# Kernel optimization log

Hardware: AMD Instinct MI355X
Metric: run time of the kernel (lower is better)

The kernel has to match this reference:

```python
import jax, jax.numpy as jnp
import numpy as np

N = 262144        # input_size = n_nodes * in_features (n_kernels = 1)
E = 16777216      # number of nonzero (i, j, param_idx) entries in weight_distribution
NPARAMS = 1280    # in_features * n_node_labels^2 * max_distance * n_kernels
NB = 16           # in_features * n_node_labels * n_kernels


def setup_inputs() -> dict:
    key = jax.random.key(0)
    ks = jax.random.split(key, 7)
    return {
        "x": jax.random.normal(ks[0], (N,), jnp.float32),
        "Param_W": jax.random.normal(ks[1], (NPARAMS,), jnp.float32),
        "Param_b": jax.random.normal(ks[2], (NB,), jnp.float32),
        "w_rows": jax.random.randint(ks[3], (E,), 0, N, jnp.int32),
        "w_cols": jax.random.randint(ks[4], (E,), 0, N, jnp.int32),
        "w_params": jax.random.randint(ks[5], (E,), 0, NPARAMS, jnp.int32),
        "b_params": jax.random.randint(ks[6], (N,), 0, NB, jnp.int32),
    }


def reference(x, Param_W, Param_b, w_rows, w_cols, w_params, b_params):
    # Original: W[i, j] = Param_W[p] for every (i, j, p) in weight_distribution,
    # then out = W @ x + bias. Fused gather-scale-scatter avoids materializing W.
    vals = Param_W[w_params] * x[w_cols]              # [E]
    out = jax.ops.segment_sum(vals, w_rows, num_segments=N)  # [N]
    # bias[i] = Param_b[b_params[i]] (one shared bias per output position)
    return out + Param_b[b_params]
```

## Files before the change

kernel.cpp:

```cpp
#include <hip/hip_runtime.h>


#define SLICE_BITS  15
#define SLICE_SIZE  (1 << SLICE_BITS)
#define SLICES      8
#define CHUNKS      32
#define NPARAMS_MAX 2048
#define SCAN_THREADS 1024
#define SB4         4
#define VB          4

typedef float v4f __attribute__((ext_vector_type(4)));

__global__ __launch_bounds__(256) void val_kernel(
    const float* __restrict__ x, const float* __restrict__ PW, int nparams,
    const int4* __restrict__ cols4, const int4* __restrict__ params4,
    v4f* __restrict__ vals4)
{
    __shared__ float pw[NPARAMS_MAX];
    for (int j = threadIdx.x; j < nparams; j += 256) pw[j] = PW[j];
    __syncthreads();
    const int base = blockIdx.x * (256 * VB) + threadIdx.x;
    int4 c[VB], p[VB];
#pragma unroll
    for (int k = 0; k < VB; ++k) {
        c[k] = cols4[base + k * 256];
        p[k] = params4[base + k * 256];
    }
#pragma unroll
    for (int k = 0; k < VB; ++k) {
        v4f v;
        v.x = pw[p[k].x] * x[c[k].x];
        v.y = pw[p[k].y] * x[c[k].y];
        v.z = pw[p[k].z] * x[c[k].z];
        v.w = pw[p[k].w] * x[c[k].w];
        __builtin_nontemporal_store(v, &vals4[base + k * 256]);
    }
}

__global__ __launch_bounds__(SCAN_THREADS, 1) void scan4_kernel(
    const int4* __restrict__ rows4, const float4* __restrict__ vals4,
    float* __restrict__ partials, int e4_per_chunk)
{
    __shared__ float acc[SLICE_SIZE];
    const int bid = blockIdx.x;
    const int s = bid / CHUNKS;
    const int c = bid % CHUNKS;
    for (int j = threadIdx.x; j < SLICE_SIZE; j += SCAN_THREADS) acc[j] = 0.0f;
    __syncthreads();

    const int4*   rp = rows4 + (size_t)c * e4_per_chunk;
    const float4* vp = vals4 + (size_t)c * e4_per_chunk;
    const int per_thread = e4_per_chunk / SCAN_THREADS;

    int4   rA[SB4], rB[SB4];
    float4 vA[SB4], vB[SB4];

#define LOAD(dstR, dstV, b0)                                             \
    _Pragma("unroll")                                                    \
    for (int b = 0; b < SB4; ++b) {                                      \
        const int g = ((b0) + b) * SCAN_THREADS + threadIdx.x;           \
        dstR[b] = rp[g];                                                 \
        dstV[b] = vp[g];                                                 \
    }
#define PROC(rX, vX)                                                     \
    _Pragma("unroll")                                                    \
    for (int b = 0; b < SB4; ++b) {                                      \
        if ((rX[b].x >> SLICE_BITS) == s) atomicAdd(&acc[rX[b].x & (SLICE_SIZE - 1)], vX[b].x); \
        if ((rX[b].y >> SLICE_BITS) == s) atomicAdd(&acc[rX[b].y & (SLICE_SIZE - 1)], vX[b].y); \
        if ((rX[b].z >> SLICE_BITS) == s) atomicAdd(&acc[rX[b].z & (SLICE_SIZE - 1)], vX[b].z); \
        if ((rX[b].w >> SLICE_BITS) == s) atomicAdd(&acc[rX[b].w & (SLICE_SIZE - 1)], vX[b].w); \
    }

    LOAD(rA, vA, 0)
    for (int base = 0; base < per_thread; base += 2 * SB4) {
        LOAD(rB, vB, base + SB4)
        PROC(rA, vA)
        if (base + 2 * SB4 < per_thread) {
            LOAD(rA, vA, base + 2 * SB4)
        }
        PROC(rB, vB)
    }
#undef LOAD
#undef PROC
    __syncthreads();

    float* dst = partials + (size_t)bid * SLICE_SIZE;
    for (int j = threadIdx.x; j < SLICE_SIZE; j += SCAN_THREADS) dst[j] = acc[j];
}

__global__ __launch_bounds__(256) void reduce_bias_kernel(
    const float* __restrict__ partials, const float* __restrict__ Pb,
    const int* __restrict__ bp, float* __restrict__ out, int n)
{
    const int i = blockIdx.x * 256 + threadIdx.x;
    if (i >= n) return;
    const int s = i >> SLICE_BITS;
    const int j = i & (SLICE_SIZE - 1);
    const float* p = partials + ((size_t)s * CHUNKS) * SLICE_SIZE + j;
    float sum = 0.0f;
#pragma unroll
    for (int g = 0; g < CHUNKS; ++g) sum += p[(size_t)g * SLICE_SIZE];
    out[i] = sum + Pb[bp[i]];
}

#define FB_BATCH 4
__global__ __launch_bounds__(SCAN_THREADS, 1) void slice_scan_kernel(
    const float* __restrict__ x, const float* __restrict__ PW, int nparams,
    const int4* __restrict__ rows4, const int4* __restrict__ cols4,
    const int4* __restrict__ params4, float* __restrict__ partials,
    int e4_per_chunk)
{
    __shared__ float acc[SLICE_SIZE];
    __shared__ float pw_lds[NPARAMS_MAX];
    const int bid = blockIdx.x;
    const int s = bid / CHUNKS;
    const int c = bid % CHUNKS;
    for (int j = threadIdx.x; j < SLICE_SIZE; j += SCAN_THREADS) acc[j] = 0.0f;
    for (int j = threadIdx.x; j < nparams; j += SCAN_THREADS) pw_lds[j] = PW[j];
    __syncthreads();
    const int4* rp = rows4   + (size_t)c * e4_per_chunk;
    const int4* cp = cols4   + (size_t)c * e4_per_chunk;
    const int4* qp = params4 + (size_t)c * e4_per_chunk;
    const int per_thread = e4_per_chunk / SCAN_THREADS;
    for (int base = 0; base < per_thread; base += FB_BATCH) {
        int4 r[FB_BATCH], cc[FB_BATCH], pp[FB_BATCH];
#pragma unroll
        for (int b = 0; b < FB_BATCH; ++b) {
            const int g = (base + b) * SCAN_THREADS + threadIdx.x;
            r[b] = rp[g]; cc[b] = cp[g]; pp[b] = qp[g];
        }
#pragma unroll
        for (int b = 0; b < FB_BATCH; ++b) {
            if ((r[b].x >> SLICE_BITS) == s)
                atomicAdd(&acc[r[b].x & (SLICE_SIZE - 1)], pw_lds[pp[b].x] * x[cc[b].x]);
            if ((r[b].y >> SLICE_BITS) == s)
                atomicAdd(&acc[r[b].y & (SLICE_SIZE - 1)], pw_lds[pp[b].y] * x[cc[b].y]);
            if ((r[b].z >> SLICE_BITS) == s)
                atomicAdd(&acc[r[b].z & (SLICE_SIZE - 1)], pw_lds[pp[b].z] * x[cc[b].z]);
            if ((r[b].w >> SLICE_BITS) == s)
                atomicAdd(&acc[r[b].w & (SLICE_SIZE - 1)], pw_lds[pp[b].w] * x[cc[b].w]);
        }
    }
    __syncthreads();
    float* dst = partials + (size_t)bid * SLICE_SIZE;
    for (int j = threadIdx.x; j < SLICE_SIZE; j += SCAN_THREADS) dst[j] = acc[j];
}

__global__ __launch_bounds__(256) void bias_init_kernel(const float* __restrict__ Pb,
                                                        const int* __restrict__ bp,
                                                        float* __restrict__ out, int n) {
    int i = blockIdx.x * 256 + threadIdx.x;
    if (i < n) out[i] = Pb[bp[i]];
}

__global__ __launch_bounds__(256) void edge_scatter_kernel(const float* __restrict__ x,
                                                           const float* __restrict__ PW,
                                                           const int* __restrict__ rows,
                                                           const int* __restrict__ cols,
                                                           const int* __restrict__ params,
                                                           float* __restrict__ out, int E) {
    int e = blockIdx.x * 256 + threadIdx.x;
    if (e < E) atomicAdd(out + rows[e], PW[params[e]] * x[cols[e]]);
}

extern "C" void kernel_launch(void* const* d_in, const int* in_sizes, int n_in,
                              void* d_out, int out_size, void* d_ws, size_t ws_size,
                              hipStream_t stream) {
    const float* x        = (const float*)d_in[0];
    const float* Param_W  = (const float*)d_in[1];
    const float* Param_b  = (const float*)d_in[2];
    const int*   w_rows   = (const int*)d_in[3];
    const int*   w_cols   = (const int*)d_in[4];
    const int*   w_params = (const int*)d_in[5];
    const int*   b_params = (const int*)d_in[6];
    float* out = (float*)d_out;

    const int N_  = in_sizes[0];
    const int NP_ = in_sizes[1];
    const int E_  = in_sizes[3];
    const int e4  = E_ / 4;

    const size_t partial_bytes = (size_t)SLICES * CHUNKS * SLICE_SIZE * sizeof(float);
    const size_t vals_bytes    = (size_t)E_ * sizeof(float);
    const bool shapes_ok = (N_ == SLICES * SLICE_SIZE) && (NP_ <= NPARAMS_MAX) &&
                           (E_ % (4 * 256 * VB) == 0) &&
                           (E_ % (4 * CHUNKS * SCAN_THREADS * 2 * SB4) == 0);

    if (shapes_ok && ws_size >= vals_bytes + partial_bytes) {
        float*  vals     = (float*)d_ws;
        float*  partials = (float*)((char*)d_ws + vals_bytes);
        const int e4_per_chunk = e4 / CHUNKS;
        val_kernel<<<e4 / (256 * VB), 256, 0, stream>>>(
            x, Param_W, NP_, (const int4*)w_cols, (const int4*)w_params, (v4f*)vals);
        scan4_kernel<<<SLICES * CHUNKS, SCAN_THREADS, 0, stream>>>(
            (const int4*)w_rows, (const float4*)vals, partials, e4_per_chunk);
        reduce_bias_kernel<<<(N_ + 255) / 256, 256, 0, stream>>>(
            partials, Param_b, b_params, out, N_);
    } else if ((N_ == SLICES * SLICE_SIZE) && (NP_ <= NPARAMS_MAX) &&
               (E_ % (4 * CHUNKS * SCAN_THREADS * FB_BATCH) == 0) &&
               ws_size >= partial_bytes) {
        float* partials = (float*)d_ws;
        const int e4_per_chunk = e4 / CHUNKS;
        slice_scan_kernel<<<SLICES * CHUNKS, SCAN_THREADS, 0, stream>>>(
            x, Param_W, NP_, (const int4*)w_rows, (const int4*)w_cols,
            (const int4*)w_params, partials, e4_per_chunk);
        reduce_bias_kernel<<<(N_ + 255) / 256, 256, 0, stream>>>(
            partials, Param_b, b_params, out, N_);
    } else {
        bias_init_kernel<<<(N_ + 255) / 256, 256, 0, stream>>>(Param_b, b_params, out, N_);
        edge_scatter_kernel<<<(E_ + 255) / 256, 256, 0, stream>>>(
            x, Param_W, w_rows, w_cols, w_params, out, E_);
    }
}
```

Baseline: 330.4 us.

## Overlap second-half value computation with first-half slice scan in merged kernel

Splits the edge list in half. The first half's values are computed by val_kernel. A merged kernel then has half its threads scan the first half into shared-memory slice accumulators while the other half computes values for the second half, and scan4_kernel finishes the second half by accumulating into the partials. The aim is to hide the val_kernel's gather and memory traffic behind the scan's LDS atomics. The cost is an extra read-modify-write of the partials buffer and an extra kernel launch, and the merged kernel reads PW from global memory instead of shared.

```diff
diff --git a/kernel.cpp b/kernel.cpp
--- a/kernel.cpp
+++ b/kernel.cpp
@@ -9,6 +9,9 @@
 #define SCAN_THREADS 1024
 #define SB4         4
 #define VB          4
+#define M_SCAN_T    512
+#define M_VAL_T     512
+#define M_THREADS   1024
 
 typedef float v4f __attribute__((ext_vector_type(4)));
 
@@ -40,7 +43,7 @@
 
 __global__ __launch_bounds__(SCAN_THREADS, 1) void scan4_kernel(
     const int4* __restrict__ rows4, const float4* __restrict__ vals4,
-    float* __restrict__ partials, int e4_per_chunk)
+    float* __restrict__ partials, int e4_per_chunk, int accumulate)
 {
     __shared__ float acc[SLICE_SIZE];
     const int bid = blockIdx.x;
@@ -59,7 +62,7 @@
 #define LOAD(dstR, dstV, b0)                                             \
     _Pragma("unroll")                                                    \
     for (int b = 0; b < SB4; ++b) {                                      \
-        const int g = ((b0) + b) * SCAN_THREADS + threadIdx.x;           \
+        const int g = ((b0) + b) * SCAN_THREADS + (int)threadIdx.x;      \
         dstR[b] = rp[g];                                                 \
         dstV[b] = vp[g];                                                 \
     }
@@ -86,7 +89,89 @@
     __syncthreads();
 
     float* dst = partials + (size_t)bid * SLICE_SIZE;
-    for (int j = threadIdx.x; j < SLICE_SIZE; j += SCAN_THREADS) dst[j] = acc[j];
+    if (accumulate) {
+        for (int j = threadIdx.x; j < SLICE_SIZE; j += SCAN_THREADS) dst[j] += acc[j];
+    } else {
+        for (int j = threadIdx.x; j < SLICE_SIZE; j += SCAN_THREADS) dst[j] = acc[j];
+    }
+}
+
+__global__ __launch_bounds__(M_THREADS, 1) void merged_kernel(
+    const int4* __restrict__ rows4, const float4* __restrict__ vals4,
+    float* __restrict__ partials, int e4_per_chunk,
+    const float* __restrict__ x, const float* __restrict__ PW,
+    const int4* __restrict__ cols4v, const int4* __restrict__ params4v,
+    v4f* __restrict__ vals4v, int vpt)
+{
+    __shared__ float acc[SLICE_SIZE];
+    const int bid = blockIdx.x;
+    const int s = bid / CHUNKS;
+    const int c = bid % CHUNKS;
+    for (int j = threadIdx.x; j < SLICE_SIZE; j += M_THREADS) acc[j] = 0.0f;
+    __syncthreads();
+
+    if (threadIdx.x < M_SCAN_T) {
+        const int4*   rp = rows4 + (size_t)c * e4_per_chunk;
+        const float4* vp = vals4 + (size_t)c * e4_per_chunk;
+        const int per_thread = e4_per_chunk / M_SCAN_T;
+
+        int4   rA[SB4], rB[SB4];
+        float4 vA[SB4], vB[SB4];
+
+#define MLOAD(dstR, dstV, b0)                                            \
+    _Pragma("unroll")                                                    \
+    for (int b = 0; b < SB4; ++b) {                                      \
+        const int g = ((b0) + b) * M_SCAN_T + (int)threadIdx.x;          \
+        dstR[b] = rp[g];                                                 \
+        dstV[b] = vp[g];                                                 \
+    }
+#define MPROC(rX, vX)                                                    \
+    _Pragma("unroll")                                                    \
+    for (int b = 0; b < SB4; ++b) {                                      \
+        if ((rX[b].x >> SLICE_BITS) == s) atomicAdd(&acc[rX[b].x & (SLICE_SIZE - 1)], vX[b].x); \
+        if ((rX[b].y >> SLICE_BITS) == s) atomicAdd(&acc[rX[b].y & (SLICE_SIZE - 1)], vX[b].y); \
+        if ((rX[b].z >> SLICE_BITS) == s) atomicAdd(&acc[rX[b].z & (SLICE_SIZE - 1)], vX[b].z); \
+        if ((rX[b].w >> SLICE_BITS) == s) atomicAdd(&acc[rX[b].w & (SLICE_SIZE - 1)], vX[b].w); \
+    }
+
+        MLOAD(rA, vA, 0)
+        for (int base = 0; base < per_thread; base += 2 * SB4) {
+            MLOAD(rB, vB, base + SB4)
+            MPROC(rA, vA)
+            if (base + 2 * SB4 < per_thread) {
+                MLOAD(rA, vA, base + 2 * SB4)
+            }
+            MPROC(rB, vB)
+        }
+#undef MLOAD
+#undef MPROC
+    } else {
+        const int vtid = (int)threadIdx.x - M_SCAN_T;
+        const size_t blockBase = (size_t)bid * vpt * M_VAL_T;
+        for (int k = 0; k < vpt; k += 4) {
+            int4 cc[4], pp[4];
+#pragma unroll
+            for (int u = 0; u < 4; ++u) {
+                const size_t g = blockBase + (size_t)(k + u) * M_VAL_T + vtid;
+                cc[u] = cols4v[g];
+                pp[u] = params4v[g];
+            }
+#pragma unroll
+            for (int u = 0; u < 4; ++u) {
+                const size_t g = blockBase + (size_t)(k + u) * M_VAL_T + vtid;
+                v4f v;
+                v.x = PW[pp[u].x] * x[cc[u].x];
+                v.y = PW[pp[u].y] * x[cc[u].y];
+                v.z = PW[pp[u].z] * x[cc[u].z];
+                v.w = PW[pp[u].w] * x[cc[u].w];
+                __builtin_nontemporal_store(v, &vals4v[g]);
+            }
+        }
+    }
+    __syncthreads();
+
+    float* dst = partials + (size_t)bid * SLICE_SIZE;
+    for (int j = threadIdx.x; j < SLICE_SIZE; j += M_THREADS) dst[j] = acc[j];
 }
 
 __global__ __launch_bounds__(256) void reduce_bias_kernel(
@@ -180,25 +265,52 @@
     const int NP_ = in_sizes[1];
     const int E_  = in_sizes[3];
     const int e4  = E_ / 4;
+    const int e4h = e4 / 2;
 
     const size_t partial_bytes = (size_t)SLICES * CHUNKS * SLICE_SIZE * sizeof(float);
     const size_t vals_bytes    = (size_t)E_ * sizeof(float);
-    const bool shapes_ok = (N_ == SLICES * SLICE_SIZE) && (NP_ <= NPARAMS_MAX) &&
-                           (E_ % (4 * 256 * VB) == 0) &&
-                           (E_ % (4 * CHUNKS * SCAN_THREADS * 2 * SB4) == 0);
-
-    if (shapes_ok && ws_size >= vals_bytes + partial_bytes) {
+
+    const bool base_ok = (N_ == SLICES * SLICE_SIZE) && (NP_ <= NPARAMS_MAX);
+
+    bool split_ok = base_ok && (E_ % 8 == 0) && (e4h % CHUNKS == 0) &&
+                    (e4h % (256 * VB) == 0);
+    const int e4c_h = split_ok ? (e4h / CHUNKS) : 0;
+    const int vpt   = split_ok ? (e4h / (256 * M_VAL_T)) : 0;
+    split_ok = split_ok &&
+               (e4c_h % (M_SCAN_T * 2 * SB4) == 0) &&
+               (e4c_h % (SCAN_THREADS * 2 * SB4) == 0) &&
+               (vpt > 0) && (vpt % 4 == 0) &&
+               ((size_t)256 * M_VAL_T * vpt == (size_t)e4h);
+
+    const bool full_ok = base_ok && (E_ % (4 * 256 * VB) == 0) &&
+                         (E_ % (4 * CHUNKS * SCAN_THREADS * 2 * SB4) == 0);
+
+    if (split_ok && ws_size >= vals_bytes + partial_bytes) {
+        float* vals     = (float*)d_ws;
+        float* partials = (float*)((char*)d_ws + vals_bytes);
+
+        val_kernel<<<e4h / (256 * VB), 256, 0, stream>>>(
+            x, Param_W, NP_, (const int4*)w_cols, (const int4*)w_params, (v4f*)vals);
+        merged_kernel<<<SLICES * CHUNKS, M_THREADS, 0, stream>>>(
+            (const int4*)w_rows, (const float4*)vals, partials, e4c_h,
+            x, Param_W,
+            (const int4*)w_cols + e4h, (const int4*)w_params + e4h,
+            (v4f*)vals + e4h, vpt);
+        scan4_kernel<<<SLICES * CHUNKS, SCAN_THREADS, 0, stream>>>(
+            (const int4*)w_rows + e4h, (const float4*)vals + e4h, partials, e4c_h, 1);
+        reduce_bias_kernel<<<(N_ + 255) / 256, 256, 0, stream>>>(
+            partials, Param_b, b_params, out, N_);
+    } else if (full_ok && ws_size >= vals_bytes + partial_bytes) {
         float*  vals     = (float*)d_ws;
         float*  partials = (float*)((char*)d_ws + vals_bytes);
         const int e4_per_chunk = e4 / CHUNKS;
         val_kernel<<<e4 / (256 * VB), 256, 0, stream>>>(
             x, Param_W, NP_, (const int4*)w_cols, (const int4*)w_params, (v4f*)vals);
         scan4_kernel<<<SLICES * CHUNKS, SCAN_THREADS, 0, stream>>>(
-            (const int4*)w_rows, (const float4*)vals, partials, e4_per_chunk);
+            (const int4*)w_rows, (const float4*)vals, partials, e4_per_chunk, 0);
         reduce_bias_kernel<<<(N_ + 255) / 256, 256, 0, stream>>>(
             partials, Param_b, b_params, out, N_);
-    } else if ((N_ == SLICES * SLICE_SIZE) && (NP_ <= NPARAMS_MAX) &&
-               (E_ % (4 * CHUNKS * SCAN_THREADS * FB_BATCH) == 0) &&
+    } else if (base_ok && (E_ % (4 * CHUNKS * SCAN_THREADS * FB_BATCH) == 0) &&
                ws_size >= partial_bytes) {
         float* partials = (float*)d_ws;
         const int e4_per_chunk = e4 / CHUNKS;
```

Measured after the change: 353.0 us. 6.9% more time.

## Fuse value gather into slice scan with software-pipelined predicated gathers

Applied to the files above, without the earlier changes.

Replaces the val_kernel + scan4 pipeline with a single fused scan kernel that streams rows/cols/params, gathers x and Param_W only for edges whose row falls in the block's slice, and double-buffers the stream/gather/atomic stages. This removes writing and re-reading the E-sized vals array and the separate kernel launch. In exchange, each of the 8 slice blocks per chunk re-reads cols and params (three index streams instead of rows+vals), and the register pressure from double buffering is high.

```diff
diff --git a/kernel.cpp b/kernel.cpp
--- a/kernel.cpp
+++ b/kernel.cpp
@@ -12,6 +12,76 @@
 
 typedef float v4f __attribute__((ext_vector_type(4)));
 
+__global__ __launch_bounds__(SCAN_THREADS, 1) void fused_scan_kernel(
+    const float* __restrict__ x, const float* __restrict__ PW,
+    const int4* __restrict__ rows4, const int4* __restrict__ cols4,
+    const int4* __restrict__ params4, float* __restrict__ partials,
+    int e4_per_chunk)
+{
+    __shared__ float acc[SLICE_SIZE];
+    const int bid = blockIdx.x;
+    const int s = bid / CHUNKS;
+    const int c = bid % CHUNKS;
+    const int tid = threadIdx.x;
+    for (int j = tid; j < SLICE_SIZE; j += SCAN_THREADS) acc[j] = 0.0f;
+    __syncthreads();
+
+    const int4* rp = rows4   + (size_t)c * e4_per_chunk;
+    const int4* cp = cols4   + (size_t)c * e4_per_chunk;
+    const int4* qp = params4 + (size_t)c * e4_per_chunk;
+    const int per_thread = e4_per_chunk / SCAN_THREADS;
+    const int nb = per_thread / SB4;
+
+    int4   sr0[SB4], sc0[SB4], sp0[SB4];
+    int4   sr1[SB4], sc1[SB4], sp1[SB4];
+    int4   r0[SB4],  r1[SB4];
+    float4 gx0[SB4], gp0[SB4];
+    float4 gx1[SB4], gp1[SB4];
+
+#define FSTREAM(K, b0)                                                       \
+    _Pragma("unroll")                                                        \
+    for (int b = 0; b < SB4; ++b) {                                          \
+        const int g = ((b0) * SB4 + b) * SCAN_THREADS + tid;                 \
+        sr##K[b] = rp[g]; sc##K[b] = cp[g]; sp##K[b] = qp[g];                \
+    }
+#define FGATHER(K)                                                           \
+    _Pragma("unroll")                                                        \
+    for (int b = 0; b < SB4; ++b) {                                          \
+        r##K[b] = sr##K[b];                                                  \
+        if ((sr##K[b].x >> SLICE_BITS) == s) { gx##K[b].x = x[sc##K[b].x]; gp##K[b].x = PW[sp##K[b].x]; } \
+        if ((sr##K[b].y >> SLICE_BITS) == s) { gx##K[b].y = x[sc##K[b].y]; gp##K[b].y = PW[sp##K[b].y]; } \
+        if ((sr##K[b].z >> SLICE_BITS) == s) { gx##K[b].z = x[sc##K[b].z]; gp##K[b].z = PW[sp##K[b].z]; } \
+        if ((sr##K[b].w >> SLICE_BITS) == s) { gx##K[b].w = x[sc##K[b].w]; gp##K[b].w = PW[sp##K[b].w]; } \
+    }
+#define FADD(K)                                                              \
+    _Pragma("unroll")                                                        \
+    for (int b = 0; b < SB4; ++b) {                                          \
+        if ((r##K[b].x >> SLICE_BITS) == s) atomicAdd(&acc[r##K[b].x & (SLICE_SIZE - 1)], gx##K[b].x * gp##K[b].x); \
+        if ((r##K[b].y >> SLICE_BITS) == s) atomicAdd(&acc[r##K[b].y & (SLICE_SIZE - 1)], gx##K[b].y * gp##K[b].y); \
+        if ((r##K[b].z >> SLICE_BITS) == s) atomicAdd(&acc[r##K[b].z & (SLICE_SIZE - 1)], gx##K[b].z * gp##K[b].z); \
+        if ((r##K[b].w >> SLICE_BITS) == s) atomicAdd(&acc[r##K[b].w & (SLICE_SIZE - 1)], gx##K[b].w * gp##K[b].w); \
+    }
+
+    FSTREAM(0, 0)
+    FSTREAM(1, 1)
+    FGATHER(0)
+    for (int j = 0; j < nb; j += 2) {
+        if (j + 2 < nb) { FSTREAM(0, j + 2) }
+        FGATHER(1)
+        FADD(0)
+        if (j + 3 < nb) { FSTREAM(1, j + 3) }
+        if (j + 2 < nb) { FGATHER(0) }
+        FADD(1)
+    }
+#undef FSTREAM
+#undef FGATHER
+#undef FADD
+
+    __syncthreads();
+    float* dst = partials + (size_t)bid * SLICE_SIZE;
+    for (int j = tid; j < SLICE_SIZE; j += SCAN_THREADS) dst[j] = acc[j];
+}
+
 __global__ __launch_bounds__(256) void val_kernel(
     const float* __restrict__ x, const float* __restrict__ PW, int nparams,
     const int4* __restrict__ cols4, const int4* __restrict__ params4,
@@ -59,7 +129,7 @@
 #define LOAD(dstR, dstV, b0)                                             \
     _Pragma("unroll")                                                    \
     for (int b = 0; b < SB4; ++b) {                                      \
-        const int g = ((b0) + b) * SCAN_THREADS + threadIdx.x;           \
+        const int g = ((b0) + b) * SCAN_THREADS + (int)threadIdx.x;      \
         dstR[b] = rp[g];                                                 \
         dstV[b] = vp[g];                                                 \
     }
@@ -102,49 +172,6 @@
 #pragma unroll
     for (int g = 0; g < CHUNKS; ++g) sum += p[(size_t)g * SLICE_SIZE];
     out[i] = sum + Pb[bp[i]];
-}
-
-#define FB_BATCH 4
-__global__ __launch_bounds__(SCAN_THREADS, 1) void slice_scan_kernel(
-    const float* __restrict__ x, const float* __restrict__ PW, int nparams,
-    const int4* __restrict__ rows4, const int4* __restrict__ cols4,
-    const int4* __restrict__ params4, float* __restrict__ partials,
-    int e4_per_chunk)
-{
-    __shared__ float acc[SLICE_SIZE];
-    __shared__ float pw_lds[NPARAMS_MAX];
-    const int bid = blockIdx.x;
-    const int s = bid / CHUNKS;
-    const int c = bid % CHUNKS;
-    for (int j = threadIdx.x; j < SLICE_SIZE; j += SCAN_THREADS) acc[j] = 0.0f;
-    for (int j = threadIdx.x; j < nparams; j += SCAN_THREADS) pw_lds[j] = PW[j];
-    __syncthreads();
-    const int4* rp = rows4   + (size_t)c * e4_per_chunk;
-    const int4* cp = cols4   + (size_t)c * e4_per_chunk;
-    const int4* qp = params4 + (size_t)c * e4_per_chunk;
-    const int per_thread = e4_per_chunk / SCAN_THREADS;
-    for (int base = 0; base < per_thread; base += FB_BATCH) {
-        int4 r[FB_BATCH], cc[FB_BATCH], pp[FB_BATCH];
-#pragma unroll
-        for (int b = 0; b < FB_BATCH; ++b) {
-            const int g = (base + b) * SCAN_THREADS + threadIdx.x;
-            r[b] = rp[g]; cc[b] = cp[g]; pp[b] = qp[g];
-        }
-#pragma unroll
-        for (int b = 0; b < FB_BATCH; ++b) {
-            if ((r[b].x >> SLICE_BITS) == s)
-                atomicAdd(&acc[r[b].x & (SLICE_SIZE - 1)], pw_lds[pp[b].x] * x[cc[b].x]);
-            if ((r[b].y >> SLICE_BITS) == s)
-                atomicAdd(&acc[r[b].y & (SLICE_SIZE - 1)], pw_lds[pp[b].y] * x[cc[b].y]);
-            if ((r[b].z >> SLICE_BITS) == s)
-                atomicAdd(&acc[r[b].z & (SLICE_SIZE - 1)], pw_lds[pp[b].z] * x[cc[b].z]);
-            if ((r[b].w >> SLICE_BITS) == s)
-                atomicAdd(&acc[r[b].w & (SLICE_SIZE - 1)], pw_lds[pp[b].w] * x[cc[b].w]);
-        }
-    }
-    __syncthreads();
-    float* dst = partials + (size_t)bid * SLICE_SIZE;
-    for (int j = threadIdx.x; j < SLICE_SIZE; j += SCAN_THREADS) dst[j] = acc[j];
 }
 
 __global__ __launch_bounds__(256) void bias_init_kernel(const float* __restrict__ Pb,
@@ -183,11 +210,23 @@
 
     const size_t partial_bytes = (size_t)SLICES * CHUNKS * SLICE_SIZE * sizeof(float);
     const size_t vals_bytes    = (size_t)E_ * sizeof(float);
-    const bool shapes_ok = (N_ == SLICES * SLICE_SIZE) && (NP_ <= NPARAMS_MAX) &&
-                           (E_ % (4 * 256 * VB) == 0) &&
-                           (E_ % (4 * CHUNKS * SCAN_THREADS * 2 * SB4) == 0);
-
-    if (shapes_ok && ws_size >= vals_bytes + partial_bytes) {
+
+    const bool base_ok = (N_ == SLICES * SLICE_SIZE) && (NP_ <= NPARAMS_MAX);
+
+    const bool fused_ok = base_ok && (e4 % CHUNKS == 0) &&
+                          ((e4 / CHUNKS) % (SCAN_THREADS * 2 * SB4) == 0);
+    const bool full_ok = base_ok && (E_ % (4 * 256 * VB) == 0) &&
+                         (E_ % (4 * CHUNKS * SCAN_THREADS * 2 * SB4) == 0);
+
+    if (fused_ok && ws_size >= partial_bytes) {
+        float* partials = (float*)d_ws;
+        const int e4_per_chunk = e4 / CHUNKS;
+        fused_scan_kernel<<<SLICES * CHUNKS, SCAN_THREADS, 0, stream>>>(
+            x, Param_W, (const int4*)w_rows, (const int4*)w_cols,
+            (const int4*)w_params, partials, e4_per_chunk);
+        reduce_bias_kernel<<<(N_ + 255) / 256, 256, 0, stream>>>(
+            partials, Param_b, b_params, out, N_);
+    } else if (full_ok && ws_size >= vals_bytes + partial_bytes) {
         float*  vals     = (float*)d_ws;
         float*  partials = (float*)((char*)d_ws + vals_bytes);
         const int e4_per_chunk = e4 / CHUNKS;
@@ -197,16 +236,6 @@
             (const int4*)w_rows, (const float4*)vals, partials, e4_per_chunk);
         reduce_bias_kernel<<<(N_ + 255) / 256, 256, 0, stream>>>(
             partials, Param_b, b_params, out, N_);
-    } else if ((N_ == SLICES * SLICE_SIZE) && (NP_ <= NPARAMS_MAX) &&
-               (E_ % (4 * CHUNKS * SCAN_THREADS * FB_BATCH) == 0) &&
-               ws_size >= partial_bytes) {
-        float* partials = (float*)d_ws;
-        const int e4_per_chunk = e4 / CHUNKS;
-        slice_scan_kernel<<<SLICES * CHUNKS, SCAN_THREADS, 0, stream>>>(
-            x, Param_W, NP_, (const int4*)w_rows, (const int4*)w_cols,
-            (const int4*)w_params, partials, e4_per_chunk);
-        reduce_bias_kernel<<<(N_ + 255) / 256, 256, 0, stream>>>(
-            partials, Param_b, b_params, out, N_);
     } else {
         bias_init_kernel<<<(N_ + 255) / 256, 256, 0, stream>>>(Param_b, b_params, out, N_);
         edge_scatter_kernel<<<(E_ + 255) / 256, 256, 0, stream>>>(
```

Result: slower. 832.1 us (+151.9%).

## Replace slice-scan partial reduction with direct global atomic scatter

Applied to the files above, without the earlier changes.

Swaps the three-stage pipeline (value precompute, per-slice LDS scan over all edges, partial reduction) for a bias-init kernel followed by one fused kernel. That kernel gathers Param_W from LDS and x from global memory, then does global float atomicAdd into the output. This drops the 8x rescanning of row indices and the partials traffic, but relies on 16M global atomics spread randomly over 1 MB of output. It also makes the result order-nondeterministic. The old fallback slice_scan kernel is deleted.

```diff
diff --git a/kernel.cpp b/kernel.cpp
--- a/kernel.cpp
+++ b/kernel.cpp
@@ -12,6 +12,43 @@
 
 typedef float v4f __attribute__((ext_vector_type(4)));
 
+__global__ __launch_bounds__(256) void scatter_atomic_kernel(
+    const float* __restrict__ x, const float* __restrict__ PW, int nparams,
+    const int4* __restrict__ rows4, const int4* __restrict__ cols4,
+    const int4* __restrict__ params4, float* __restrict__ out)
+{
+    __shared__ float pw[NPARAMS_MAX];
+    for (int j = threadIdx.x; j < nparams; j += 256) pw[j] = PW[j];
+    __syncthreads();
+
+    const int base = blockIdx.x * (256 * VB) + threadIdx.x;
+    int4 r[VB], c[VB], p[VB];
+#pragma unroll
+    for (int k = 0; k < VB; ++k) {
+        r[k] = rows4[base + k * 256];
+        c[k] = cols4[base + k * 256];
+        p[k] = params4[base + k * 256];
+    }
+#pragma unroll
+    for (int k = 0; k < VB; ++k) {
+        float vx = pw[p[k].x] * x[c[k].x];
+        float vy = pw[p[k].y] * x[c[k].y];
+        float vz = pw[p[k].z] * x[c[k].z];
+        float vw = pw[p[k].w] * x[c[k].w];
+        atomicAdd(&out[r[k].x], vx);
+        atomicAdd(&out[r[k].y], vy);
+        atomicAdd(&out[r[k].z], vz);
+        atomicAdd(&out[r[k].w], vw);
+    }
+}
+
+__global__ __launch_bounds__(256) void bias_init_kernel(const float* __restrict__ Pb,
+                                                        const int* __restrict__ bp,
+                                                        float* __restrict__ out, int n) {
+    int i = blockIdx.x * 256 + threadIdx.x;
+    if (i < n) out[i] = Pb[bp[i]];
+}
+
 __global__ __launch_bounds__(256) void val_kernel(
     const float* __restrict__ x, const float* __restrict__ PW, int nparams,
     const int4* __restrict__ cols4, const int4* __restrict__ params4,
@@ -59,7 +96,7 @@
 #define LOAD(dstR, dstV, b0)                                             \
     _Pragma("unroll")                                                    \
     for (int b = 0; b < SB4; ++b) {                                      \
-        const int g = ((b0) + b) * SCAN_THREADS + threadIdx.x;           \
+        const int g = ((b0) + b) * SCAN_THREADS + (int)threadIdx.x;      \
         dstR[b] = rp[g];                                                 \
         dstV[b] = vp[g];                                                 \
     }
@@ -102,56 +139,6 @@
 #pragma unroll
     for (int g = 0; g < CHUNKS; ++g) sum += p[(size_t)g * SLICE_SIZE];
     out[i] = sum + Pb[bp[i]];
-}
-
-#define FB_BATCH 4
-__global__ __launch_bounds__(SCAN_THREADS, 1) void slice_scan_kernel(
-    const float* __restrict__ x, const float* __restrict__ PW, int nparams,
-    const int4* __restrict__ rows4, const int4* __restrict__ cols4,
-    const int4* __restrict__ params4, float* __restrict__ partials,
-    int e4_per_chunk)
-{
-    __shared__ float acc[SLICE_SIZE];
-    __shared__ float pw_lds[NPARAMS_MAX];
-    const int bid = blockIdx.x;
-    const int s = bid / CHUNKS;
-    const int c = bid % CHUNKS;
-    for (int j = threadIdx.x; j < SLICE_SIZE; j += SCAN_THREADS) acc[j] = 0.0f;
-    for (int j = threadIdx.x; j < nparams; j += SCAN_THREADS) pw_lds[j] = PW[j];
-    __syncthreads();
-    const int4* rp = rows4   + (size_t)c * e4_per_chunk;
-    const int4* cp = cols4   + (size_t)c * e4_per_chunk;
-    const int4* qp = params4 + (size_t)c * e4_per_chunk;
-    const int per_thread = e4_per_chunk / SCAN_THREADS;
-    for (int base = 0; base < per_thread; base += FB_BATCH) {
-        int4 r[FB_BATCH], cc[FB_BATCH], pp[FB_BATCH];
-#pragma unroll
-        for (int b = 0; b < FB_BATCH; ++b) {
-            const int g = (base + b) * SCAN_THREADS + threadIdx.x;
-            r[b] = rp[g]; cc[b] = cp[g]; pp[b] = qp[g];
-        }
-#pragma unroll
-        for (int b = 0; b < FB_BATCH; ++b) {
-            if ((r[b].x >> SLICE_BITS) == s)
-                atomicAdd(&acc[r[b].x & (SLICE_SIZE - 1)], pw_lds[pp[b].x] * x[cc[b].x]);
-            if ((r[b].y >> SLICE_BITS) == s)
-                atomicAdd(&acc[r[b].y & (SLICE_SIZE - 1)], pw_lds[pp[b].y] * x[cc[b].y]);
-            if ((r[b].z >> SLICE_BITS) == s)
-                atomicAdd(&acc[r[b].z & (SLICE_SIZE - 1)], pw_lds[pp[b].z] * x[cc[b].z]);
-            if ((r[b].w >> SLICE_BITS) == s)
-                atomicAdd(&acc[r[b].w & (SLICE_SIZE - 1)], pw_lds[pp[b].w] * x[cc[b].w]);
-        }
-    }
-    __syncthreads();
-    float* dst = partials + (size_t)bid * SLICE_SIZE;
-    for (int j = threadIdx.x; j < SLICE_SIZE; j += SCAN_THREADS) dst[j] = acc[j];
-}
-
-__global__ __launch_bounds__(256) void bias_init_kernel(const float* __restrict__ Pb,
-                                                        const int* __restrict__ bp,
-                                                        float* __restrict__ out, int n) {
-    int i = blockIdx.x * 256 + threadIdx.x;
-    if (i < n) out[i] = Pb[bp[i]];
 }
 
 __global__ __launch_bounds__(256) void edge_scatter_kernel(const float* __restrict__ x,
@@ -183,11 +170,19 @@
 
     const size_t partial_bytes = (size_t)SLICES * CHUNKS * SLICE_SIZE * sizeof(float);
     const size_t vals_bytes    = (size_t)E_ * sizeof(float);
-    const bool shapes_ok = (N_ == SLICES * SLICE_SIZE) && (NP_ <= NPARAMS_MAX) &&
-                           (E_ % (4 * 256 * VB) == 0) &&
-                           (E_ % (4 * CHUNKS * SCAN_THREADS * 2 * SB4) == 0);
-
-    if (shapes_ok && ws_size >= vals_bytes + partial_bytes) {
+
+    const bool base_ok = (N_ == SLICES * SLICE_SIZE) && (NP_ <= NPARAMS_MAX);
+
+    const bool scatter_ok = (NP_ <= NPARAMS_MAX) && (E_ % (4 * 256 * VB) == 0);
+    const bool full_ok = base_ok && (E_ % (4 * 256 * VB) == 0) &&
+                         (E_ % (4 * CHUNKS * SCAN_THREADS * 2 * SB4) == 0);
+
+    if (scatter_ok) {
+        bias_init_kernel<<<(N_ + 255) / 256, 256, 0, stream>>>(Param_b, b_params, out, N_);
+        scatter_atomic_kernel<<<e4 / (256 * VB), 256, 0, stream>>>(
+            x, Param_W, NP_, (const int4*)w_rows, (const int4*)w_cols,
+            (const int4*)w_params, out);
+    } else if (full_ok && ws_size >= vals_bytes + partial_bytes) {
         float*  vals     = (float*)d_ws;
         float*  partials = (float*)((char*)d_ws + vals_bytes);
         const int e4_per_chunk = e4 / CHUNKS;
@@ -197,16 +192,6 @@
             (const int4*)w_rows, (const float4*)vals, partials, e4_per_chunk);
         reduce_bias_kernel<<<(N_ + 255) / 256, 256, 0, stream>>>(
             partials, Param_b, b_params, out, N_);
-    } else if ((N_ == SLICES * SLICE_SIZE) && (NP_ <= NPARAMS_MAX) &&
-               (E_ % (4 * CHUNKS * SCAN_THREADS * FB_BATCH) == 0) &&
-               ws_size >= partial_bytes) {
-        float* partials = (float*)d_ws;
-        const int e4_per_chunk = e4 / CHUNKS;
-        slice_scan_kernel<<<SLICES * CHUNKS, SCAN_THREADS, 0, stream>>>(
-            x, Param_W, NP_, (const int4*)w_rows, (const int4*)w_cols,
-            (const int4*)w_params, partials, e4_per_chunk);
-        reduce_bias_kernel<<<(N_ + 255) / 256, 256, 0, stream>>>(
-            partials, Param_b, b_params, out, N_);
     } else {
         bias_init_kernel<<<(N_ + 255) / 256, 256, 0, stream>>>(Param_b, b_params, out, N_);
         edge_scatter_kernel<<<(E_ + 255) / 256, 256, 0, stream>>>(
```

Result: slower. 949.6 us (+187.4%).
